# Optimization experiments

Measured on AMD Instinct MI355X. Metric: run time of the kernel, lower is better.

The kernel has to match this reference:

```python
import jax, jax.numpy as jnp
import numpy as np

KERNEL_SIZE = 9   # temporal window Gamma (odd)
STRIDE = 1        # temporal stride; fifo_size = STRIDE*(K-1)+1
NUM_PARTITIONS = 3


def setup_inputs() -> dict:
    key = jax.random.key(0)
    k1, k2, k3, k4 = jax.random.split(key, 4)
    x = jax.random.normal(k1, (16, 64, 2048, 25), dtype=jnp.float32)         # (N, C_in, L, V)
    A = jax.random.uniform(k2, (3, 25, 25), dtype=jnp.float32)                # (P, V, V)
    conv_w = jax.random.normal(k3, (192, 64), dtype=jnp.float32) * 0.05       # (C_out*P, C_in) 1x1 conv
    conv_b = jax.random.normal(k4, (192,), dtype=jnp.float32) * 0.05
    return {"x": x, "A": A, "conv_w": conv_w, "conv_b": conv_b}


def reference(x, A, conv_w, conv_b):
    # x: (N, C_in, L, V); A: (P, V, V)
    N, C_in, L, V = x.shape
    P = A.shape[0]
    C_out = conv_w.shape[0] // P

    # residual: in_channels == out_channels and stride == 1 -> identity
    res = x

    # 1x1 conv over (L, V): pointwise channel mix
    a = jnp.einsum('nclv,oc->nolv', x, conv_w) + conv_b[None, :, None, None]  # (N, C_out*P, L, V)
    a = a.reshape(N, P, C_out, L, V)

    # per-partition adjacency matmul, summed over partitions (the FIFO loop
    # sums over partitions anyway, so the partition reduction fuses here)
    es = jnp.einsum('npclv,pvw->nlcw', a, A)  # (N, L, C_out, V)

    # FIFO windowed temporal sum: out[t] = sum_{k=0}^{K-1} es[t - k*STRIDE]
    # (frames before t=0 are zeros in the FIFO)
    pad = (KERNEL_SIZE - 1) * STRIDE
    padded = jnp.pad(es, ((0, 0), (pad, 0), (0, 0), (0, 0)))
    h = padded[:, 0:L]
    for j in range(1, KERNEL_SIZE):
        h = h + padded[:, j * STRIDE:j * STRIDE + L]
    h = jnp.transpose(h, (0, 2, 1, 3))  # (N, C_out, L, V)

    return jax.nn.relu(h + res)
```

## Files before the change

kernel.cpp:

```cpp
#include <hip/hip_runtime.h>

namespace {
constexpr int kL    = 2048;
constexpr int kV    = 25;
constexpr int kTL   = 8;
constexpr int kXsC  = kL * kV;
constexpr long kXsN = 64L * kXsC;

typedef __attribute__((ext_vector_type(8)))  short bf16x8;
typedef __attribute__((ext_vector_type(16))) float f32x16;

__device__ __forceinline__ float b2f(unsigned short u) {
  union { unsigned u32; float f; } x; x.u32 = ((unsigned)u) << 16; return x.f;
}
__device__ __forceinline__ unsigned short f2b(float f) {
  union { float f; unsigned u; } x; x.f = f;
  unsigned r = x.u + 0x7FFF + ((x.u >> 16) & 1);
  return (unsigned short)(r >> 16);
}
__device__ __forceinline__ unsigned cvt_pk(float lo, float hi) {
  unsigned r;
  asm("v_cvt_pk_bf16_f32 %0, %1, %2" : "=v"(r) : "v"(lo), "v"(hi));
  return r;
}
}

__global__ void stgcn_pre(const float* __restrict__ A,
                          const float* __restrict__ cw,
                          const float* __restrict__ cb,
                          unsigned short* __restrict__ wsu) {
  int tid = blockIdx.x * 256 + threadIdx.x;
  int nthr = gridDim.x * 256;
  for (int i = tid; i < 2 * 12 * 64 * 8; i += nthr) {
    int j = i & 7, lane = (i >> 3) & 63;
    int rem = i >> 9;
    int kg = rem % 12, mt2 = rem / 12;
    int c  = 32 * mt2 + (lane & 31);
    int p  = kg >> 2, ksl = kg & 3;
    int ci = 16 * ksl + 8 * (lane >> 5) + j;
    wsu[i] = f2b(cw[(p * 64 + c) * 64 + ci]);
  }
  for (int i = tid; i < 3 * 2 * 64 * 8; i += nthr) {
    int j = i & 7, lane = (i >> 3) & 63, ks = (i >> 9) & 1, p = i >> 10;
    int w = lane & 31;
    int v = 16 * ks + 8 * (lane >> 5) + j;
    float val = (v < kV && w < kV) ? A[(p * kV + v) * kV + w] : 0.f;
    wsu[12288 + i] = f2b(val);
  }
  float* bias2 = (float*)((char*)wsu + 30720);
  for (int i = tid; i < 64 * kV; i += nthr) {
    int c = i / kV, w = i % kV;
    float s = 0.f;
    for (int p = 0; p < 3; ++p) {
      float as = 0.f;
      for (int v = 0; v < kV; ++v) as += A[(p * kV + v) * kV + w];
      s += cb[p * 64 + c] * as;
    }
    bias2[i] = s;
  }
}

__global__ __launch_bounds__(512, 4)
void stgcn_main(const float* __restrict__ x,
                const unsigned short* __restrict__ wsu,
                float* __restrict__ out) {
  __shared__ unsigned short sBuf[20480];

  const int t    = threadIdx.x;
  const int lane = t & 63;
  const int wid  = t >> 6;
  const int hi   = lane >> 5;
  const int l31  = lane & 31;

  const int b   = blockIdx.x + (int)gridDim.x * blockIdx.y;
  const int w_  = (b & 7) * 512 + (b >> 3);
  const int lt  = w_ & 255;
  const int nb  = w_ >> 8;
  const int l0  = lt * kTL;

  const float* xn = x + (long)nb * kXsN;
  float* outn     = out + (long)nb * kXsN;
  const float* bias2 = (const float*)((const char*)wsu + 30720);

  {
    const int ci = t >> 3, q = t & 7;
    const int rowb = ci * 8 * 40;
    if (q == 7) {
      const int c4 = ((3 ^ (ci & 3)) << 3) | 4;
      uint2 z = {0u, 0u};
      #pragma unroll
      for (int dl = 0; dl < 8; ++dl) *(uint2*)&sBuf[rowb + dl * 40 + c4] = z;
    } else {
      const int colL = 4 * q;
      const int c4 = (((colL >> 3) ^ (ci & 3)) << 3) | (colL & 7);
      const float* xr = xn + (long)ci * kXsC + (long)(l0 - 8) * kV + colL;
      const bool full = (q < 6);
      float a0 = 0.f, a1 = 0.f, a2 = 0.f, a3 = 0.f;
      if (l0) {
        #pragma unroll
        for (int j = 0; j < 9; ++j) {
          const float* r = xr + j * kV;
          a0 += r[0];
          if (full) { a1 += r[1]; a2 += r[2]; a3 += r[3]; }
        }
      } else {
        const float* r = xr + 8 * kV;
        a0 = r[0];
        if (full) { a1 = r[1]; a2 = r[2]; a3 = r[3]; }
      }
      #pragma unroll
      for (int dl = 0; dl < 8; ++dl) {
        uint2 o = { cvt_pk(a0, a1), cvt_pk(a2, a3) };
        *(uint2*)&sBuf[rowb + dl * 40 + c4] = o;
        if (dl < 7) {
          const float* pn = xr + (dl + 9) * kV;
          a0 += pn[0];
          if (full) { a1 += pn[1]; a2 += pn[2]; a3 += pn[3]; }
          if (l0) {
            const float* po = xr + dl * kV;
            a0 -= po[0];
            if (full) { a1 -= po[1]; a2 -= po[2]; a3 -= po[3]; }
          }
        }
      }
    }
  }
  __syncthreads();

  bf16x8 af[2][2];
  #pragma unroll
  for (int mtl = 0; mtl < 2; ++mtl) {
    const int m  = 32 * (2 * wid + mtl) + l31;
    const int cia = m >> 3;
    #pragma unroll
    for (int ks = 0; ks < 2; ++ks) {
      const int vblk = 2 * ks + hi;
      af[mtl][ks] = *(const bf16x8*)&sBuf[m * 40 + ((vblk ^ (cia & 3)) << 3)];
    }
  }
  __syncthreads();


  const int mt2 = wid & 1;
  const int ng  = wid >> 1;
  const int nnt = (ng < 3) ? 2 : 1;
  const int nt0 = (ng < 3) ? 2 * ng : 6;

  f32x16 acc[2];
  #pragma unroll
  for (int q = 0; q < 2; ++q)
    #pragma unroll
    for (int r = 0; r < 16; ++r) acc[q][r] = 0.f;

  const bool wok = (l31 < kV);

  #define S1(p) {                                                             \
    _Pragma("unroll")                                                         \
    for (int mtl = 0; mtl < 2; ++mtl) {                                       \
      f32x16 cz;                                                              \
      _Pragma("unroll")                                                       \
      for (int r = 0; r < 16; ++r) cz[r] = 0.f;                               \
      _Pragma("unroll")                                                       \
      for (int ks = 0; ks < 2; ++ks) {                                        \
        bf16x8 bfr = *(const bf16x8*)&wsu[12288 + (((p) * 2 + ks) * 64 + lane) * 8]; \
        cz = __builtin_amdgcn_mfma_f32_32x32x16_bf16(af[mtl][ks], bfr, cz, 0, 0, 0); \
      }                                                                       \
      if (wok) {                                                              \
        _Pragma("unroll")                                                     \
        for (int r = 0; r < 16; ++r) {                                        \
          const int mo = (r & 3) + 8 * (r >> 2) + 4 * hi;                     \
          const int m  = 32 * (2 * wid + mtl) + mo;                           \
          const int ci = m >> 3;                                              \
          const int nidx = (m & 7) * kV + l31;                                \
          sBuf[nidx * 64 + (((ci >> 3) ^ (nidx & 7)) << 3) + (ci & 7)] =      \
              (unsigned short)cvt_pk(cz[r], cz[r]);                           \
        }                                                                     \
      }                                                                       \
    }                                                                         \
  }

  #define S2(p) {                                                             \
    _Pragma("unroll")                                                         \
    for (int ksl = 0; ksl < 4; ++ksl) {                                       \
      bf16x8 wf = *(const bf16x8*)&wsu[((mt2 * 12 + (p) * 4 + ksl) * 64 + lane) * 8]; \
      _Pragma("unroll")                                                       \
      for (int q = 0; q < 2; ++q) {                                           \
        if (q < nnt) {                                                        \
          const int nidx = 32 * (nt0 + q) + l31;                              \
          const int o = 2 * ksl + hi;                                         \
          bf16x8 yf = *(const bf16x8*)&sBuf[nidx * 64 + ((o ^ (nidx & 7)) << 3)]; \
          acc[q] = __builtin_amdgcn_mfma_f32_32x32x16_bf16(wf, yf, acc[q], 0, 0, 0); \
        }                                                                     \
      }                                                                       \
    }                                                                         \
  }

  S1(0); __syncthreads();
  S2(0); __syncthreads();
  S1(1); __syncthreads();
  S2(1); __syncthreads();
  S1(2); __syncthreads();
  S2(2);

  #undef S1
  #undef S2

  __syncthreads();

  {
    const long xb = (long)l0 * kV;
    #pragma unroll
    for (int k = 0; k < 25; ++k) {
      const int i = t + 512 * k;
      const int c = i / 200, rem = i - 200 * c;
      const int l = rem / 25, wv = rem - 25 * l;
      const float xv = xn[(long)c * kXsC + xb + rem];
      const float cnt = lt ? 9.f : (float)(l + 1);
      sBuf[i] = f2b(fmaf(cnt, bias2[c * kV + wv], xv));
    }
  }
  __syncthreads();

  #pragma unroll
  for (int q = 0; q < 2; ++q) {
    if (q < nnt) {
      const int nidx = 32 * (nt0 + q) + l31;
      if (nidx < 200) {
        const int dl = nidx / 25, wv = nidx - 25 * dl;
        const long base = (long)(l0 + dl) * kV + wv;
        #pragma unroll
        for (int r = 0; r < 16; ++r) {
          const int c = 32 * mt2 + (r & 3) + 8 * (r >> 2) + 4 * hi;
          float val = acc[q][r] + b2f(sBuf[c * 200 + nidx]);
          outn[(long)c * kXsC + base] = fmaxf(val, 0.f);
        }
      }
    }
  }
}

extern "C" void kernel_launch(void* const* d_in, const int* in_sizes, int n_in,
                              void* d_out, int out_size, void* d_ws, size_t ws_size,
                              hipStream_t stream) {
  const float* x  = (const float*)d_in[0];
  const float* A  = (const float*)d_in[1];
  const float* cw = (const float*)d_in[2];
  const float* cb = (const float*)d_in[3];
  unsigned short* wsu = (unsigned short*)d_ws;

  hipLaunchKernelGGL(stgcn_pre, dim3(8), dim3(256), 0, stream, A, cw, cb, wsu);
  hipLaunchKernelGGL(stgcn_main, dim3(kL / kTL, 16), dim3(512), 0, stream,
                     x, wsu, (float*)d_out);
}
```

Measured before the change: 221.5 us.

## Halve temporal tile to four frames with 256-thread blocks and rewritten window prefix

Reduces the per-block temporal tile from 8 to 4 frames, halving block size, shared memory and MFMA work per block and doubling the grid to 8192 one-dimensional blocks. Each thread in the prologue now loads 8 contiguous vertex columns and builds the windowed sum by accumulating up to 8 preceding frames and then sliding, replacing the fixed 9-frame unrolled prefix. The aim is higher occupancy and better latency hiding on a memory-bound kernel. In exchange, the 8 halo frames are now reloaded for only 4 output frames, so redundant reads of x per output roughly double, and the halo loop is no longer unrolled.

```diff
diff --git a/kernel.cpp b/kernel.cpp
--- a/kernel.cpp
+++ b/kernel.cpp
@@ -3,7 +3,7 @@
 namespace {
 constexpr int kL    = 2048;
 constexpr int kV    = 25;
-constexpr int kTL   = 8;
+constexpr int kTL   = 4;
 constexpr int kXsC  = kL * kV;
 constexpr long kXsN = 64L * kXsC;
 
@@ -60,11 +60,11 @@
   }
 }
 
-__global__ __launch_bounds__(512, 4)
+__global__ __launch_bounds__(256, 8)
 void stgcn_main(const float* __restrict__ x,
                 const unsigned short* __restrict__ wsu,
                 float* __restrict__ out) {
-  __shared__ unsigned short sBuf[20480];
+  __shared__ unsigned short sBuf[10240];
 
   const int t    = threadIdx.x;
   const int lane = t & 63;
@@ -72,10 +72,10 @@
   const int hi   = lane >> 5;
   const int l31  = lane & 31;
 
-  const int b   = blockIdx.x + (int)gridDim.x * blockIdx.y;
-  const int w_  = (b & 7) * 512 + (b >> 3);
-  const int lt  = w_ & 255;
-  const int nb  = w_ >> 8;
+  const int b   = blockIdx.x;
+  const int w_  = (b & 7) * 1024 + (b >> 3);
+  const int lt  = w_ & 511;
+  const int nb  = w_ >> 9;
   const int l0  = lt * kTL;
 
   const float* xn = x + (long)nb * kXsN;
@@ -83,45 +83,47 @@
   const float* bias2 = (const float*)((const char*)wsu + 30720);
 
   {
-    const int ci = t >> 3, q = t & 7;
-    const int rowb = ci * 8 * 40;
-    if (q == 7) {
-      const int c4 = ((3 ^ (ci & 3)) << 3) | 4;
-      uint2 z = {0u, 0u};
+    const int ciA = t >> 2, qA = t & 3;
+    const int rowb = ciA * 4 * 40;
+    const int octet = (qA ^ (ciA & 3)) << 3;
+    const float* xcol = xn + (long)ciA * kXsC + 8 * qA;
+    const bool sub = (l0 >= 8);
+
+    if (qA < 3) {
+      float a0=0.f,a1=0.f,a2=0.f,a3=0.f,a4=0.f,a5=0.f,a6=0.f,a7=0.f;
+      if (l0) {
+        const int jlo = sub ? l0 - 8 : 0;
+        for (int j = jlo; j < l0; ++j) {
+          const float* r = xcol + (long)j * kV;
+          a0+=r[0]; a1+=r[1]; a2+=r[2]; a3+=r[3];
+          a4+=r[4]; a5+=r[5]; a6+=r[6]; a7+=r[7];
+        }
+      }
       #pragma unroll
-      for (int dl = 0; dl < 8; ++dl) *(uint2*)&sBuf[rowb + dl * 40 + c4] = z;
+      for (int dl = 0; dl < kTL; ++dl) {
+        const float* rn = xcol + (long)(l0 + dl) * kV;
+        a0+=rn[0]; a1+=rn[1]; a2+=rn[2]; a3+=rn[3];
+        a4+=rn[4]; a5+=rn[5]; a6+=rn[6]; a7+=rn[7];
+        uint4 o = { cvt_pk(a0,a1), cvt_pk(a2,a3), cvt_pk(a4,a5), cvt_pk(a6,a7) };
+        *(uint4*)&sBuf[rowb + dl * 40 + octet] = o;
+        if (sub) {
+          const float* ro = xcol + (long)(l0 + dl - 8) * kV;
+          a0-=ro[0]; a1-=ro[1]; a2-=ro[2]; a3-=ro[3];
+          a4-=ro[4]; a5-=ro[5]; a6-=ro[6]; a7-=ro[7];
+        }
+      }
     } else {
-      const int colL = 4 * q;
-      const int c4 = (((colL >> 3) ^ (ci & 3)) << 3) | (colL & 7);
-      const float* xr = xn + (long)ci * kXsC + (long)(l0 - 8) * kV + colL;
-      const bool full = (q < 6);
-      float a0 = 0.f, a1 = 0.f, a2 = 0.f, a3 = 0.f;
+      float a0 = 0.f;
       if (l0) {
-        #pragma unroll
-        for (int j = 0; j < 9; ++j) {
-          const float* r = xr + j * kV;
-          a0 += r[0];
-          if (full) { a1 += r[1]; a2 += r[2]; a3 += r[3]; }
-        }
-      } else {
-        const float* r = xr + 8 * kV;
-        a0 = r[0];
-        if (full) { a1 = r[1]; a2 = r[2]; a3 = r[3]; }
+        const int jlo = sub ? l0 - 8 : 0;
+        for (int j = jlo; j < l0; ++j) a0 += xcol[(long)j * kV];
       }
       #pragma unroll
-      for (int dl = 0; dl < 8; ++dl) {
-        uint2 o = { cvt_pk(a0, a1), cvt_pk(a2, a3) };
-        *(uint2*)&sBuf[rowb + dl * 40 + c4] = o;
-        if (dl < 7) {
-          const float* pn = xr + (dl + 9) * kV;
-          a0 += pn[0];
-          if (full) { a1 += pn[1]; a2 += pn[2]; a3 += pn[3]; }
-          if (l0) {
-            const float* po = xr + dl * kV;
-            a0 -= po[0];
-            if (full) { a1 -= po[1]; a2 -= po[2]; a3 -= po[3]; }
-          }
-        }
+      for (int dl = 0; dl < kTL; ++dl) {
+        a0 += xcol[(long)(l0 + dl) * kV];
+        uint4 o = { cvt_pk(a0, 0.f), 0u, 0u, 0u };
+        *(uint4*)&sBuf[rowb + dl * 40 + octet] = o;
+        if (sub) a0 -= xcol[(long)(l0 + dl - 8) * kV];
       }
     }
   }
@@ -130,8 +132,8 @@
   bf16x8 af[2][2];
   #pragma unroll
   for (int mtl = 0; mtl < 2; ++mtl) {
-    const int m  = 32 * (2 * wid + mtl) + l31;
-    const int cia = m >> 3;
+    const int m   = 32 * (2 * wid + mtl) + l31;
+    const int cia = m >> 2;
     #pragma unroll
     for (int ks = 0; ks < 2; ++ks) {
       const int vblk = 2 * ks + hi;
@@ -140,11 +142,8 @@
   }
   __syncthreads();
 
-
   const int mt2 = wid & 1;
   const int ng  = wid >> 1;
-  const int nnt = (ng < 3) ? 2 : 1;
-  const int nt0 = (ng < 3) ? 2 * ng : 6;
 
   f32x16 acc[2];
   #pragma unroll
@@ -170,8 +169,8 @@
         for (int r = 0; r < 16; ++r) {                                        \
           const int mo = (r & 3) + 8 * (r >> 2) + 4 * hi;                     \
           const int m  = 32 * (2 * wid + mtl) + mo;                           \
-          const int ci = m >> 3;                                              \
-          const int nidx = (m & 7) * kV + l31;                                \
+          const int ci = m >> 2;                                              \
+          const int nidx = (m & 3) * kV + l31;                                \
           sBuf[nidx * 64 + (((ci >> 3) ^ (nidx & 7)) << 3) + (ci & 7)] =      \
               (unsigned short)cvt_pk(cz[r], cz[r]);                           \
         }                                                                     \
@@ -185,12 +184,10 @@
       bf16x8 wf = *(const bf16x8*)&wsu[((mt2 * 12 + (p) * 4 + ksl) * 64 + lane) * 8]; \
       _Pragma("unroll")                                                       \
       for (int q = 0; q < 2; ++q) {                                           \
-        if (q < nnt) {                                                        \
-          const int nidx = 32 * (nt0 + q) + l31;                              \
-          const int o = 2 * ksl + hi;                                         \
-          bf16x8 yf = *(const bf16x8*)&sBuf[nidx * 64 + ((o ^ (nidx & 7)) << 3)]; \
-          acc[q] = __builtin_amdgcn_mfma_f32_32x32x16_bf16(wf, yf, acc[q], 0, 0, 0); \
-        }                                                                     \
+        const int nidx = 32 * (2 * ng + q) + l31;                             \
+        const int o = 2 * ksl + hi;                                           \
+        bf16x8 yf = *(const bf16x8*)&sBuf[nidx * 64 + ((o ^ (nidx & 7)) << 3)]; \
+        acc[q] = __builtin_amdgcn_mfma_f32_32x32x16_bf16(wf, yf, acc[q], 0, 0, 0); \
       }                                                                       \
     }                                                                         \
   }
@@ -211,11 +208,11 @@
     const long xb = (long)l0 * kV;
     #pragma unroll
     for (int k = 0; k < 25; ++k) {
-      const int i = t + 512 * k;
-      const int c = i / 200, rem = i - 200 * c;
-      const int l = rem / 25, wv = rem - 25 * l;
+      const int i = t + 256 * k;
+      const int c = i / 100, rem = i - 100 * c;
+      const int dl = rem / 25, wv = rem - 25 * dl;
       const float xv = xn[(long)c * kXsC + xb + rem];
-      const float cnt = lt ? 9.f : (float)(l + 1);
+      const float cnt = fminf((float)(l0 + dl + 1), 9.f);
       sBuf[i] = f2b(fmaf(cnt, bias2[c * kV + wv], xv));
     }
   }
@@ -223,17 +220,14 @@
 
   #pragma unroll
   for (int q = 0; q < 2; ++q) {
-    if (q < nnt) {
-      const int nidx = 32 * (nt0 + q) + l31;
-      if (nidx < 200) {
-        const int dl = nidx / 25, wv = nidx - 25 * dl;
-        const long base = (long)(l0 + dl) * kV + wv;
-        #pragma unroll
-        for (int r = 0; r < 16; ++r) {
-          const int c = 32 * mt2 + (r & 3) + 8 * (r >> 2) + 4 * hi;
-          float val = acc[q][r] + b2f(sBuf[c * 200 + nidx]);
-          outn[(long)c * kXsC + base] = fmaxf(val, 0.f);
-        }
+    const int nidx = 32 * (2 * ng + q) + l31;
+    if (nidx < 100) {
+      const long base = (long)l0 * kV + nidx;
+      #pragma unroll
+      for (int r = 0; r < 16; ++r) {
+        const int c = 32 * mt2 + (r & 3) + 8 * (r >> 2) + 4 * hi;
+        float val = acc[q][r] + b2f(sBuf[c * 100 + nidx]);
+        outn[(long)c * kXsC + base] = fmaxf(val, 0.f);
       }
     }
   }
@@ -249,6 +243,6 @@
   unsigned short* wsu = (unsigned short*)d_ws;
 
   hipLaunchKernelGGL(stgcn_pre, dim3(8), dim3(256), 0, stream, A, cw, cb, wsu);
-  hipLaunchKernelGGL(stgcn_main, dim3(kL / kTL, 16), dim3(512), 0, stream,
+  hipLaunchKernelGGL(stgcn_main, dim3((kL / kTL) * 16), dim3(256), 0, stream,
                      x, wsu, (float*)d_out);
 }
```

Measured after the change: 463.8 us. 2.09x slower.
